# Performance work log

Hardware: AMD Instinct MI355X
Metric: run time of the kernel (lower is better)

The kernel has to match this reference:

```python
import jax, jax.numpy as jnp
import numpy as np

S, N, D, F = 32, 128, 256, 516
TRI = (N - 1) * N // 2  # fact(n-1) = n(n-1)/2 lower-triangular edge slots


def _mlp_readout(y, W0, b0, W1, b1, W2, b2):
    # standard MLPReadout with L=2 halving layers + final linear
    y = jax.nn.relu(y @ W0.T + b0)
    y = jax.nn.relu(y @ W1.T + b1)
    return y @ W2.T + b2


def _gru(xs, h0, Wih, Whh, bih, bhh):
    # xs: (S, T, Din); torch.nn.GRUCell math, scanned over time
    def step(h, x_t):
        gi = x_t @ Wih.T + bih
        gh = h @ Whh.T + bhh
        i_r, i_z, i_n = jnp.split(gi, 3, axis=-1)
        h_r, h_z, h_n = jnp.split(gh, 3, axis=-1)
        r = jax.nn.sigmoid(i_r + h_r)
        z = jax.nn.sigmoid(i_z + h_z)
        n = jnp.tanh(i_n + r * h_n)
        h_new = (1.0 - z) * n + z * h
        return h_new, h_new
    _, out = jax.lax.scan(step, h0, jnp.swapaxes(xs, 0, 1))
    return jnp.swapaxes(out, 0, 1)  # (S, T, D)


def setup_inputs() -> dict:
    key = jax.random.key(0)
    ks = jax.random.split(key, 16)
    def nrm(k, shape, s=0.05):
        return (jax.random.normal(k, shape) * s).astype(jnp.float32)
    return {
        'x': jax.random.uniform(ks[0], (S, N, F), dtype=jnp.float32),
        'con': jax.random.uniform(ks[1], (S, TRI, 2), dtype=jnp.float32),
        'z_ph': jax.random.uniform(ks[2], (D,), minval=-1.0, maxval=1.0, dtype=jnp.float32),
        'init_ph': jax.random.uniform(ks[3], (D,), minval=-1.0, maxval=1.0, dtype=jnp.float32),
        'cc_W0': nrm(ks[4], (D, 2 * D)), 'cc_b0': jnp.zeros((D,), jnp.float32),
        'cc_W1': nrm(ks[5], (D // 2, D)), 'cc_b1': jnp.zeros((D // 2,), jnp.float32),
        'cc_W2': nrm(ks[6], (D, D // 2)), 'cc_b2': jnp.zeros((D,), jnp.float32),
        'er_W0': nrm(ks[7], (D, 2 * D)), 'er_b0': jnp.zeros((D,), jnp.float32),
        'er_W1': nrm(ks[8], (D // 2, D)), 'er_b1': jnp.zeros((D // 2,), jnp.float32),
        'er_W2': nrm(ks[9], (2, D // 2)), 'er_b2': jnp.zeros((2,), jnp.float32),
        'rr_W': nrm(ks[10], (D, F)), 'rr_b': jnp.zeros((D,), jnp.float32),
        'dec_Wih': nrm(ks[11], (3 * D, D)), 'dec_Whh': nrm(ks[12], (3 * D, D)),
        'dec_bih': jnp.zeros((3 * D,), jnp.float32), 'dec_bhh': jnp.zeros((3 * D,), jnp.float32),
        'upd_Wih': nrm(ks[13], (3 * D, D)), 'upd_Whh': nrm(ks[14], (3 * D, D)),
        'upd_bih': jnp.zeros((3 * D,), jnp.float32), 'upd_bhh': jnp.zeros((3 * D,), jnp.float32),
    }


def reference(x, con, z_ph, init_ph, cc_W0, cc_b0, cc_W1, cc_b1, cc_W2, cc_b2,
              er_W0, er_b0, er_W1, er_b1, er_W2, er_b2, rr_W, rr_b,
              dec_Wih, dec_Whh, dec_bih, dec_bhh, upd_Wih, upd_Whh, upd_bih, upd_bhh):
    Sb = x.shape[0]
    Nm1 = x.shape[1] - 1
    # initial content = compact_content([z ; init]) (same for every sample)
    c0 = _mlp_readout(jnp.concatenate([z_ph, init_ph])[None, :],
                      cc_W0, cc_b0, cc_W1, cc_b1, cc_W2, cc_b2)
    c0 = jnp.broadcast_to(c0, (Sb, D))
    # update-model input stream depends only on data x[:, 1:] -> precompute
    rnninp = jax.nn.relu(jnp.einsum('snf,df->snd', x[:, 1:], rr_W) + rr_b)  # (S, N-1, D)
    h0 = jnp.zeros((Sb, D), x.dtype)
    u_out = _gru(rnninp, h0, upd_Wih, upd_Whh, upd_bih, upd_bhh)            # (S, N-1, D)
    # decoder consumes content0 then the first N-2 update outputs
    content_seq = jnp.concatenate([c0[:, None], u_out[:, :-1]], axis=1)     # (S, N-1, D)
    mem = _gru(content_seq, h0, dec_Wih, dec_Whh, dec_bih, dec_bhh)         # (S, N-1, D)
    # step i emits edges (j, i) for j <= i; flatten lower triangle (static indices)
    i_idx = np.repeat(np.arange(Nm1), np.arange(1, Nm1 + 1))
    j_idx = np.concatenate([np.arange(i + 1) for i in range(Nm1)])
    edge_rep = jnp.concatenate([mem[:, j_idx], mem[:, i_idx]], axis=-1)     # (S, TRI, 2D)
    logits = _mlp_readout(edge_rep, er_W0, er_b0, er_W1, er_b1, er_W2, er_b2)
    p = jax.nn.softmax(logits, axis=-1)                                     # (S, TRI, 2)
    # F.binary_cross_entropy with torch's log clamp at -100
    bce = -(con * jnp.clip(jnp.log(p), -100.0, None)
            + (1.0 - con) * jnp.clip(jnp.log1p(-p), -100.0, None))
    return jnp.sum(bce, axis=1)  # (S, 2) negative log-likelihood per class slot
```

## Files before the change

kernel.cpp:

```cpp
#include <hip/hip_runtime.h>
#include <cstddef>

#define S_ 32
#define NM1 127
#define D_ 256
#define F_ 516
#define TRI_ 8128
#define G_ 768
#define M_ (S_ * NM1)

typedef __bf16 v8bf __attribute__((ext_vector_type(8)));
typedef __bf16 bf2 __attribute__((ext_vector_type(2)));
typedef float v4f __attribute__((ext_vector_type(4)));

#if __has_builtin(__builtin_amdgcn_fdot2_f32_bf16)
#define HAS_DOT2 1
#else
#define HAS_DOT2 0
#endif

__device__ __forceinline__ unsigned short f2bf(float f) {
    unsigned int u = __float_as_uint(f);
    unsigned int r = (u + 0x7FFFu + ((u >> 16) & 1u)) >> 16;
    return (unsigned short)r;
}

__device__ __forceinline__ void store4bf(unsigned short* p, float4 v) {
    ushort4 q;
    q.x = f2bf(v.x); q.y = f2bf(v.y); q.z = f2bf(v.z); q.w = f2bf(v.w);
    *(ushort4*)p = q;
}

__device__ __forceinline__ bf2 u2bf2(unsigned int u) {
    union { unsigned int u; bf2 v; } x; x.u = u; return x.v;
}

__device__ __forceinline__ float bflo(unsigned int u) { return __uint_as_float(u << 16); }
__device__ __forceinline__ float bfhi(unsigned int u) { return __uint_as_float(u & 0xffff0000u); }

__device__ __forceinline__ float dot2bf(unsigned int w, unsigned int hh, float acc) {
#if HAS_DOT2
    return __builtin_amdgcn_fdot2_f32_bf16(u2bf2(w), u2bf2(hh), acc, false);
#else
    return acc + bflo(w) * bflo(hh) + bfhi(w) * bfhi(hh);
#endif
}

__device__ __forceinline__ float sigmoidf_(float x) { return 1.f / (1.f + __expf(-x)); }

__device__ __forceinline__ float fast_tanh(float x) {
    float ax = fabsf(x);
    float e = __expf(2.f * ax);
    float t = 1.f - 2.f / (e + 1.f);
    return copysignf(t, x);
}

__global__ __launch_bounds__(1024) void c0_kernel(
    const float* __restrict__ z_ph, const float* __restrict__ init_ph,
    const float* __restrict__ W0, const float* __restrict__ b0,
    const float* __restrict__ W1, const float* __restrict__ b1,
    const float* __restrict__ W2, const float* __restrict__ b2,
    float* __restrict__ c0_out, float* __restrict__ out_zero)
{
    __shared__ float v[512];
    __shared__ float h0[256];
    __shared__ float h1[128];
    __shared__ float red[4][256];
    __shared__ float red1[8][128];
    const int t = threadIdx.x;
    if (t < 512) v[t] = (t < 256) ? z_ph[t] : init_ph[t - 256];
    if (t < 64) out_zero[t] = 0.f;
    __syncthreads();
    {
        int row = t & 255, part = t >> 8;
        const float* w = W0 + (size_t)row * 512 + part * 128;
        const float* vv = v + part * 128;
        float a = 0.f;
        for (int k = 0; k < 128; ++k) a += w[k] * vv[k];
        red[part][row] = a;
    }
    __syncthreads();
    if (t < 256) {
        float a = b0[t] + red[0][t] + red[1][t] + red[2][t] + red[3][t];
        h0[t] = fmaxf(a, 0.f);
    }
    __syncthreads();
    {
        int row = t & 127, part = t >> 7;
        const float* w = W1 + (size_t)row * 256 + part * 32;
        const float* vv = h0 + part * 32;
        float a = 0.f;
        for (int k = 0; k < 32; ++k) a += w[k] * vv[k];
        red1[part][row] = a;
    }
    __syncthreads();
    if (t < 128) {
        float a = b1[t];
        for (int p = 0; p < 8; ++p) a += red1[p][t];
        h1[t] = fmaxf(a, 0.f);
    }
    __syncthreads();
    {
        int row = t & 255, part = t >> 8;
        const float* w = W2 + (size_t)row * 128 + part * 32;
        const float* vv = h1 + part * 32;
        float a = 0.f;
        for (int k = 0; k < 32; ++k) a += w[k] * vv[k];
        red[part][row] = a;
    }
    __syncthreads();
    if (t < 256) c0_out[t] = b2[t] + red[0][t] + red[1][t] + red[2][t] + red[3][t];
}

__device__ __forceinline__ void do_pack(const float* __restrict__ W,
                                        unsigned int* __restrict__ wpT, int idx)
{
    if (idx >= 128 * 768) return;
    int p = idx / 768, j = idx - p * 768;
    float a = W[(size_t)j * 256 + 2 * p];
    float b = W[(size_t)j * 256 + 2 * p + 1];
    wpT[idx] = (unsigned int)f2bf(a) | ((unsigned int)f2bf(b) << 16);
}

__device__ __forceinline__ void do_cvt(const float* __restrict__ src,
                                       unsigned short* __restrict__ dst,
                                       int idx, int N, int K, int lds_, int off, int ldd)
{
    if (idx >= N * ldd) return;
    int n = idx / ldd, k = idx - n * ldd;
    float v = (k < K) ? src[(size_t)n * lds_ + off + k] : 0.f;
    dst[idx] = f2bf(v);
}

#define PREP_BLOCKS 3464

__global__ __launch_bounds__(256) void prep_all(
    const float* __restrict__ upd_Whh, unsigned int* __restrict__ wpU,
    const float* __restrict__ dec_Whh, unsigned int* __restrict__ wpD,
    const float* __restrict__ rr_W, unsigned short* __restrict__ rwbf,
    const float* __restrict__ upd_Wih, unsigned short* __restrict__ uwbf,
    const float* __restrict__ dec_Wih, unsigned short* __restrict__ dwbf,
    const float* __restrict__ er_W0, unsigned short* __restrict__ w0bf,
    const float* __restrict__ er_W1, unsigned short* __restrict__ w1bf)
{
    int bid = blockIdx.x;
    const int tid = threadIdx.x;
    if (bid < 384) { do_pack(upd_Whh, wpU, bid * 256 + tid); return; }
    bid -= 384;
    if (bid < 384) { do_pack(dec_Whh, wpD, bid * 256 + tid); return; }
    bid -= 384;
    if (bid < 520) { do_cvt(rr_W, rwbf, bid * 256 + tid, 256, 516, 516, 0, 520); return; }
    bid -= 520;
    if (bid < 768) { do_cvt(upd_Wih, uwbf, bid * 256 + tid, 768, 256, 256, 0, 256); return; }
    bid -= 768;
    if (bid < 768) { do_cvt(dec_Wih, dwbf, bid * 256 + tid, 768, 256, 256, 0, 256); return; }
    bid -= 768;
    if (bid < 256) { do_cvt(er_W0, w0bf, bid * 256 + tid, 256, 256, 512, 0, 256); return; }
    bid -= 256;
    if (bid < 256) { do_cvt(er_W0, w0bf + 256 * 256, bid * 256 + tid, 256, 256, 512, 256, 256); return; }
    bid -= 256;
    do_cvt(er_W1, w1bf, bid * 256 + tid, 128, 256, 256, 0, 256);
}

__global__ __launch_bounds__(256) void gemm_mfma(
    const float* __restrict__ A, const unsigned short* __restrict__ B,
    const float* __restrict__ bias, const float* __restrict__ c0,
    float* __restrict__ C, float* __restrict__ C2,
    int M, int N, int K, int lda, int ldb, int mode, int act, int split)
{
    __shared__ __align__(16) unsigned short As[64 * 128];
    __shared__ __align__(16) unsigned short Bs[64 * 128];
    const int tid = threadIdx.x;
    const int m0 = blockIdx.x * 64, n0 = blockIdx.y * 64;
    const int wave = tid >> 6, lane = tid & 63;
    const int lr = lane & 15, quad = lane >> 4;

    v4f acc[4];
    const v4f z4 = {0.f, 0.f, 0.f, 0.f};
#pragma unroll
    for (int nt = 0; nt < 4; ++nt) acc[nt] = z4;

    for (int k0 = 0; k0 < K; k0 += 128) {
        for (int idx = tid; idx < 64 * 32; idx += 256) {
            int r = idx >> 5, kq = idx & 31;
            int k = k0 + kq * 4;
            int m = m0 + r; if (m > M - 1) m = M - 1;
            float4 a = {0.f, 0.f, 0.f, 0.f};
            if (k < K) {
                const float* Ar;
                if (mode == 1) {
                    int ss = m / 127, tt = m - ss * 127;
                    Ar = A + (size_t)(ss * 128 + tt + 1) * lda;
                } else if (mode == 2) {
                    int tt = m % 127;
                    Ar = (tt == 0) ? c0 : (A + (size_t)(m - 1) * lda);
                } else {
                    Ar = A + (size_t)m * lda;
                }
                a = *(const float4*)&Ar[k];
            }
            store4bf(&As[r * 128 + (((kq >> 1) ^ (r & 7)) << 3) + ((kq & 1) << 2)], a);
        }
        for (int idx = tid; idx < 64 * 16; idx += 256) {
            int c = idx >> 4, kb = idx & 15;
            int k = k0 + kb * 8;
            int n = n0 + c;
            uint4 bv = {0u, 0u, 0u, 0u};
            if (k < K) bv = *(const uint4*)&B[(size_t)n * ldb + k];
            *(uint4*)&Bs[c * 128 + ((kb ^ (c & 7)) << 3)] = bv;
        }
        __syncthreads();
        const int row = wave * 16 + lr;
        const int rem = K - k0;
        const int kkm = (rem >= 128) ? 4 : ((rem + 31) >> 5);
        for (int kk = 0; kk < kkm; ++kk) {
            const v8bf af = *(const v8bf*)&As[row * 128 + ((((kk << 2) + quad) ^ (row & 7)) << 3)];
#pragma unroll
            for (int nt = 0; nt < 4; ++nt) {
                const int col = nt * 16 + lr;
                const v8bf bf = *(const v8bf*)&Bs[col * 128 + ((((kk << 2) + quad) ^ (col & 7)) << 3)];
                acc[nt] = __builtin_amdgcn_mfma_f32_16x16x32_bf16(af, bf, acc[nt], 0, 0, 0);
            }
        }
        __syncthreads();
    }
#pragma unroll
    for (int nt = 0; nt < 4; ++nt) {
        const int col = n0 + nt * 16 + lr;
#pragma unroll
        for (int r = 0; r < 4; ++r) {
            const int row = m0 + wave * 16 + quad * 4 + r;
            if (row < M) {
                float v = acc[nt][r];
                if (split) {
                    if (col < 256) C[(size_t)row * 256 + col] = v;
                    else C2[(size_t)row * 256 + (col - 256)] = v + bias[col - 256];
                } else {
                    if (bias) v += bias[col];
                    if (act) v = fmaxf(v, 0.f);
                    C[(size_t)row * N + col] = v;
                }
            }
        }
    }
}

__global__ __launch_bounds__(768, 3) void gru_scan4(
    const float* __restrict__ gi, const unsigned int* __restrict__ wpT,
    const float* __restrict__ bhh, float* __restrict__ outp, int T)
{
    const int s = blockIdx.x, j = threadIdx.x;
    __shared__ unsigned int hb[2][128];
    __shared__ float dred[768];
    __shared__ float gns[256];

    unsigned int wh[64];
#pragma unroll
    for (int p = 0; p < 64; ++p) wh[p] = wpT[p * 768 + j];

    const float bj = bhh[j];
    const float* g0 = gi + (size_t)s * T * G_;
    float* o0 = outp + (size_t)s * T * D_;
    float g_cur = g0[j];
    float h = 0.f;
    if (j < 128) { hb[0][j] = 0u; hb[1][j] = 0u; }
    __syncthreads();

    for (int t = 0; t < T; ++t) {
        float g_next = 0.f;
        if (t + 1 < T) g_next = g0[(size_t)(t + 1) * G_ + j];

        unsigned int wsb[2][16];
#pragma unroll
        for (int i = 0; i < 16; ++i) wsb[0][i] = wpT[(64 + i) * 768 + j];

        const uint4* hq4 = (const uint4*)hb[t & 1];
        float a0 = 0.f, a1 = 0.f, a2 = 0.f, a3 = 0.f;
#pragma unroll
        for (int q = 0; q < 16; ++q) {
            uint4 hv = hq4[q];
            a0 = dot2bf(wh[4 * q + 0], hv.x, a0);
            a1 = dot2bf(wh[4 * q + 1], hv.y, a1);
            a2 = dot2bf(wh[4 * q + 2], hv.z, a2);
            a3 = dot2bf(wh[4 * q + 3], hv.w, a3);
        }
#pragma unroll
        for (int c = 0; c < 4; ++c) {
            if (c + 1 < 4) {
#pragma unroll
                for (int i = 0; i < 16; ++i)
                    wsb[(c + 1) & 1][i] = wpT[(64 + (c + 1) * 16 + i) * 768 + j];
            }
            const unsigned int* wc = wsb[c & 1];
#pragma unroll
            for (int qq = 0; qq < 4; ++qq) {
                uint4 hv = hq4[16 + c * 4 + qq];
                a0 = dot2bf(wc[4 * qq + 0], hv.x, a0);
                a1 = dot2bf(wc[4 * qq + 1], hv.y, a1);
                a2 = dot2bf(wc[4 * qq + 2], hv.z, a2);
                a3 = dot2bf(wc[4 * qq + 3], hv.w, a3);
            }
        }
        float a = (a0 + a1) + (a2 + a3) + bj;
        if (j < 512) {
            dred[j] = a + g_cur;
        } else {
            dred[j] = a;
            gns[j - 512] = g_cur;
        }
        __syncthreads();
        if (j < 256) {
            const float rg = sigmoidf_(dred[j]);
            const float zg = sigmoidf_(dred[256 + j]);
            const float ng = fast_tanh(gns[j] + rg * dred[512 + j]);
            const float hnew = ng + zg * (h - ng);
            h = hnew;
            o0[(size_t)t * D_ + j] = hnew;
            const float ho = __shfl_xor(hnew, 1);
            if ((j & 1) == 0)
                hb[(t + 1) & 1][j >> 1] =
                    (unsigned int)f2bf(hnew) | ((unsigned int)f2bf(ho) << 16);
        }
        g_cur = g_next;
        __syncthreads();
    }
}

__global__ __launch_bounds__(256) void edge_kernel(
    const float* __restrict__ Amat, const float* __restrict__ Bmat,
    const unsigned short* __restrict__ w1bf, const float* __restrict__ b1,
    const float* __restrict__ W2, const float* __restrict__ b2,
    const float* __restrict__ con, float* __restrict__ out)
{
    __shared__ __align__(16) unsigned short h1s[64 * 256];
    __shared__ int ijs[128];
    __shared__ float redw[4][2];
    const int tid = threadIdx.x;
    const int s = blockIdx.y;
    const int e0 = blockIdx.x * 64;

    if (tid < 64) {
        int e = e0 + tid;
        int i = (int)((sqrtf(8.f * (float)e + 1.f) - 1.f) * 0.5f);
        while (((i + 1) * (i + 2)) / 2 <= e) ++i;
        while ((i * (i + 1)) / 2 > e) --i;
        ijs[tid * 2] = i;
        ijs[tid * 2 + 1] = e - (i * (i + 1)) / 2;
    }
    __syncthreads();

    for (int idx = tid; idx < 64 * 64; idx += 256) {
        int e = idx >> 6, k4 = idx & 63;
        int i = ijs[e * 2], j = ijs[e * 2 + 1];
        float4 a = ((const float4*)(Amat + ((size_t)s * NM1 + j) * D_))[k4];
        float4 b = ((const float4*)(Bmat + ((size_t)s * NM1 + i) * D_))[k4];
        float4 hv;
        hv.x = fmaxf(a.x + b.x, 0.f);
        hv.y = fmaxf(a.y + b.y, 0.f);
        hv.z = fmaxf(a.z + b.z, 0.f);
        hv.w = fmaxf(a.w + b.w, 0.f);
        int pc = (k4 >> 1) ^ (e & 7);
        store4bf(&h1s[e * 256 + (pc << 3) + ((k4 & 1) << 2)], hv);
    }
    __syncthreads();

    const int wave = tid >> 6, lane = tid & 63;
    const int lr = lane & 15, quad = lane >> 4;
    const int row = wave * 16 + lr;

    v4f acc[8];
    const v4f vzero = {0.f, 0.f, 0.f, 0.f};
#pragma unroll
    for (int nt = 0; nt < 8; ++nt) acc[nt] = vzero;

#pragma unroll
    for (int kt = 0; kt < 8; ++kt) {
        const int c = kt * 4 + quad;
        const int pc = c ^ (row & 7);
        const v8bf afrag = *reinterpret_cast<const v8bf*>(&h1s[row * 256 + (pc << 3)]);
        const int ko = kt * 32 + quad * 8;
#pragma unroll
        for (int nt = 0; nt < 8; ++nt) {
            const v8bf bfrag = *reinterpret_cast<const v8bf*>(&w1bf[(size_t)(nt * 16 + lr) * D_ + ko]);
            acc[nt] = __builtin_amdgcn_mfma_f32_16x16x32_bf16(afrag, bfrag, acc[nt], 0, 0, 0);
        }
    }

    float w20[8], w21[8], b1v[8];
#pragma unroll
    for (int nt = 0; nt < 8; ++nt) {
        int oc = nt * 16 + lr;
        w20[nt] = W2[oc];
        w21[nt] = W2[128 + oc];
        b1v[nt] = b1[oc];
    }
    const float cb20 = b2[0], cb21 = b2[1];
    float bsum0 = 0.f, bsum1 = 0.f;
#pragma unroll
    for (int r = 0; r < 4; ++r) {
        float l0 = 0.f, l1 = 0.f;
#pragma unroll
        for (int nt = 0; nt < 8; ++nt) {
            float h2 = fmaxf(acc[nt][r] + b1v[nt], 0.f);
            l0 += h2 * w20[nt];
            l1 += h2 * w21[nt];
        }
#pragma unroll
        for (int d = 1; d < 16; d <<= 1) {
            l0 += __shfl_xor(l0, d);
            l1 += __shfl_xor(l1, d);
        }
        if (lr == 0) {
            int e = e0 + wave * 16 + quad * 4 + r;
            l0 += cb20; l1 += cb21;
            float mx = fmaxf(l0, l1);
            float lse = mx + logf(__expf(l0 - mx) + __expf(l1 - mx));
            float lp0 = fmaxf(l0 - lse, -100.f);
            float lp1 = fmaxf(l1 - lse, -100.f);
            float c0v = con[((size_t)s * TRI_ + e) * 2];
            float c1v = con[((size_t)s * TRI_ + e) * 2 + 1];
            bsum0 -= c0v * lp0 + (1.f - c0v) * lp1;
            bsum1 -= c1v * lp1 + (1.f - c1v) * lp0;
        }
    }
#pragma unroll
    for (int d = 1; d < 64; d <<= 1) {
        bsum0 += __shfl_xor(bsum0, d);
        bsum1 += __shfl_xor(bsum1, d);
    }
    if (lane == 0) { redw[wave][0] = bsum0; redw[wave][1] = bsum1; }
    __syncthreads();
    if (tid == 0) {
        float t0 = redw[0][0] + redw[1][0] + redw[2][0] + redw[3][0];
        float t1 = redw[0][1] + redw[1][1] + redw[2][1] + redw[3][1];
        atomicAdd(&out[s * 2], t0);
        atomicAdd(&out[s * 2 + 1], t1);
    }
}

extern "C" void kernel_launch(void* const* d_in, const int* in_sizes, int n_in,
                              void* d_out, int out_size, void* d_ws, size_t ws_size,
                              hipStream_t stream)
{
    (void)in_sizes; (void)n_in; (void)out_size; (void)ws_size;
    const float* x        = (const float*)d_in[0];
    const float* con      = (const float*)d_in[1];
    const float* z_ph     = (const float*)d_in[2];
    const float* init_ph  = (const float*)d_in[3];
    const float* cc_W0    = (const float*)d_in[4];
    const float* cc_b0    = (const float*)d_in[5];
    const float* cc_W1    = (const float*)d_in[6];
    const float* cc_b1    = (const float*)d_in[7];
    const float* cc_W2    = (const float*)d_in[8];
    const float* cc_b2    = (const float*)d_in[9];
    const float* er_W0    = (const float*)d_in[10];
    const float* er_b0    = (const float*)d_in[11];
    const float* er_W1    = (const float*)d_in[12];
    const float* er_b1    = (const float*)d_in[13];
    const float* er_W2    = (const float*)d_in[14];
    const float* er_b2    = (const float*)d_in[15];
    const float* rr_W     = (const float*)d_in[16];
    const float* rr_b     = (const float*)d_in[17];
    const float* dec_Wih  = (const float*)d_in[18];
    const float* dec_Whh  = (const float*)d_in[19];
    const float* dec_bih  = (const float*)d_in[20];
    const float* dec_bhh  = (const float*)d_in[21];
    const float* upd_Wih  = (const float*)d_in[22];
    const float* upd_Whh  = (const float*)d_in[23];
    const float* upd_bih  = (const float*)d_in[24];
    const float* upd_bhh  = (const float*)d_in[25];
    float* out = (float*)d_out;

    float* ws = (float*)d_ws;
    float* c0v  = ws;
    float* gi   = ws + 256;
    float* bufA = gi + (size_t)M_ * G_;
    float* bufB = bufA + (size_t)M_ * D_;
    float* memb = bufB + (size_t)M_ * D_;
    unsigned short* w1bf = (unsigned short*)(memb + (size_t)M_ * D_);
    unsigned int* wpU = (unsigned int*)(w1bf + 128 * 256);
    unsigned int* wpD = wpU + 128 * 768;
    unsigned short* rwbf = (unsigned short*)(wpD + 128 * 768);
    unsigned short* uwbf = rwbf + 256 * 520;
    unsigned short* dwbf = uwbf + 768 * 256;
    unsigned short* w0bf = dwbf + 768 * 256;

    c0_kernel<<<1, 1024, 0, stream>>>(z_ph, init_ph, cc_W0, cc_b0, cc_W1, cc_b1,
                                      cc_W2, cc_b2, c0v, out);
    prep_all<<<PREP_BLOCKS, 256, 0, stream>>>(upd_Whh, wpU, dec_Whh, wpD,
                                              rr_W, rwbf, upd_Wih, uwbf,
                                              dec_Wih, dwbf, er_W0, w0bf,
                                              er_W1, w1bf);
    gemm_mfma<<<dim3((M_ + 63) / 64, 256 / 64), 256, 0, stream>>>(
        x, rwbf, rr_b, nullptr, bufA, nullptr, M_, 256, 516, 516, 520, 1, 1, 0);
    gemm_mfma<<<dim3((M_ + 63) / 64, 768 / 64), 256, 0, stream>>>(
        bufA, uwbf, upd_bih, nullptr, gi, nullptr, M_, 768, 256, 256, 256, 0, 0, 0);
    gru_scan4<<<S_, 768, 0, stream>>>(gi, wpU, upd_bhh, bufB, NM1);
    gemm_mfma<<<dim3((M_ + 63) / 64, 768 / 64), 256, 0, stream>>>(
        bufB, dwbf, dec_bih, c0v, gi, nullptr, M_, 768, 256, 256, 256, 2, 0, 0);
    gru_scan4<<<S_, 768, 0, stream>>>(gi, wpD, dec_bhh, memb, NM1);
    gemm_mfma<<<dim3((M_ + 63) / 64, 512 / 64), 256, 0, stream>>>(
        memb, w0bf, er_b0, nullptr, bufA, bufB, M_, 512, 256, 256, 256, 0, 0, 1);
    edge_kernel<<<dim3(TRI_ / 64, S_), 256, 0, stream>>>(
        bufA, bufB, w1bf, er_b1, er_W2, er_b2, con, out);
}
```

Measured before the change: 714.8 us.

## Use MFMA for GRU recurrent matvec with register-resident fragment-packed weights

Rewrites the per-step hidden-state matvec in the GRU scan so it uses 16x16x32 bf16 MFMA instructions instead of per-thread dot2 loops. Only row 0 of the A operand carries real data; the other rows are broadcast copies of the same hidden vector. The recurrent weights are pre-packed into MFMA B-fragment layout and kept entirely in registers (48 uint4 per lane), which removes the per-step global weight streaming of the old version. The block shrinks from 768 to 512 threads, and biases plus input gates are added in the gate stage. In exchange, most of the MFMA work is wasted on redundant rows and register pressure is high.

```diff
diff --git a/kernel.cpp b/kernel.cpp
--- a/kernel.cpp
+++ b/kernel.cpp
@@ -10,14 +10,7 @@
 #define M_ (S_ * NM1)
 
 typedef __bf16 v8bf __attribute__((ext_vector_type(8)));
-typedef __bf16 bf2 __attribute__((ext_vector_type(2)));
 typedef float v4f __attribute__((ext_vector_type(4)));
-
-#if __has_builtin(__builtin_amdgcn_fdot2_f32_bf16)
-#define HAS_DOT2 1
-#else
-#define HAS_DOT2 0
-#endif
 
 __device__ __forceinline__ unsigned short f2bf(float f) {
     unsigned int u = __float_as_uint(f);
@@ -31,19 +24,8 @@
     *(ushort4*)p = q;
 }
 
-__device__ __forceinline__ bf2 u2bf2(unsigned int u) {
-    union { unsigned int u; bf2 v; } x; x.u = u; return x.v;
-}
-
-__device__ __forceinline__ float bflo(unsigned int u) { return __uint_as_float(u << 16); }
-__device__ __forceinline__ float bfhi(unsigned int u) { return __uint_as_float(u & 0xffff0000u); }
-
-__device__ __forceinline__ float dot2bf(unsigned int w, unsigned int hh, float acc) {
-#if HAS_DOT2
-    return __builtin_amdgcn_fdot2_f32_bf16(u2bf2(w), u2bf2(hh), acc, false);
-#else
-    return acc + bflo(w) * bflo(hh) + bfhi(w) * bfhi(hh);
-#endif
+__device__ __forceinline__ v8bf u4_to_v8bf(uint4 u) {
+    union { uint4 u; v8bf v; } x; x.u = u; return x.v;
 }
 
 __device__ __forceinline__ float sigmoidf_(float x) { return 1.f / (1.f + __expf(-x)); }
@@ -112,14 +94,22 @@
     if (t < 256) c0_out[t] = b2[t] + red[0][t] + red[1][t] + red[2][t] + red[3][t];
 }
 
-__device__ __forceinline__ void do_pack(const float* __restrict__ W,
-                                        unsigned int* __restrict__ wpT, int idx)
-{
-    if (idx >= 128 * 768) return;
-    int p = idx / 768, j = idx - p * 768;
-    float a = W[(size_t)j * 256 + 2 * p];
-    float b = W[(size_t)j * 256 + 2 * p + 1];
-    wpT[idx] = (unsigned int)f2bf(a) | ((unsigned int)f2bf(b) << 16);
+__device__ __forceinline__ void do_packfrag(const float* __restrict__ W,
+                                            uint4* __restrict__ wbuf, int idx)
+{
+    if (idx >= 48 * 8 * 64) return;
+    int ct = idx >> 9;
+    int rem = idx & 511;
+    int kk = rem >> 6;
+    int lane = rem & 63;
+    int lr = lane & 15, quad = lane >> 4;
+    const float* src = W + (size_t)(ct * 16 + lr) * 256 + kk * 32 + quad * 8;
+    unsigned int wd[4];
+#pragma unroll
+    for (int i = 0; i < 4; ++i)
+        wd[i] = (unsigned int)f2bf(src[2 * i]) | ((unsigned int)f2bf(src[2 * i + 1]) << 16);
+    uint4 v; v.x = wd[0]; v.y = wd[1]; v.z = wd[2]; v.w = wd[3];
+    wbuf[idx] = v;
 }
 
 __device__ __forceinline__ void do_cvt(const float* __restrict__ src,
@@ -132,11 +122,11 @@
     dst[idx] = f2bf(v);
 }
 
-#define PREP_BLOCKS 3464
+#define PREP_BLOCKS 2888
 
 __global__ __launch_bounds__(256) void prep_all(
-    const float* __restrict__ upd_Whh, unsigned int* __restrict__ wpU,
-    const float* __restrict__ dec_Whh, unsigned int* __restrict__ wpD,
+    const float* __restrict__ upd_Whh, uint4* __restrict__ wfU,
+    const float* __restrict__ dec_Whh, uint4* __restrict__ wfD,
     const float* __restrict__ rr_W, unsigned short* __restrict__ rwbf,
     const float* __restrict__ upd_Wih, unsigned short* __restrict__ uwbf,
     const float* __restrict__ dec_Wih, unsigned short* __restrict__ dwbf,
@@ -145,10 +135,10 @@
 {
     int bid = blockIdx.x;
     const int tid = threadIdx.x;
-    if (bid < 384) { do_pack(upd_Whh, wpU, bid * 256 + tid); return; }
-    bid -= 384;
-    if (bid < 384) { do_pack(dec_Whh, wpD, bid * 256 + tid); return; }
-    bid -= 384;
+    if (bid < 96) { do_packfrag(upd_Whh, wfU, bid * 256 + tid); return; }
+    bid -= 96;
+    if (bid < 96) { do_packfrag(dec_Whh, wfD, bid * 256 + tid); return; }
+    bid -= 96;
     if (bid < 520) { do_cvt(rr_W, rwbf, bid * 256 + tid, 256, 516, 516, 0, 520); return; }
     bid -= 520;
     if (bid < 768) { do_cvt(upd_Wih, uwbf, bid * 256 + tid, 768, 256, 256, 0, 256); return; }
@@ -245,83 +235,76 @@
     }
 }
 
-__global__ __launch_bounds__(768, 3) void gru_scan4(
-    const float* __restrict__ gi, const unsigned int* __restrict__ wpT,
+__global__ __launch_bounds__(512, 2) void gru_scan6(
+    const float* __restrict__ gi, const uint4* __restrict__ wf,
     const float* __restrict__ bhh, float* __restrict__ outp, int T)
 {
-    const int s = blockIdx.x, j = threadIdx.x;
-    __shared__ unsigned int hb[2][128];
+    const int s = blockIdx.x, tid = threadIdx.x;
+    const int w = tid >> 6, lane = tid & 63;
+    const int quad = lane >> 4;
+    __shared__ unsigned int hbuf[2][128];
     __shared__ float dred[768];
-    __shared__ float gns[256];
-
-    unsigned int wh[64];
-#pragma unroll
-    for (int p = 0; p < 64; ++p) wh[p] = wpT[p * 768 + j];
-
-    const float bj = bhh[j];
+
+    uint4 wfr[6][8];
+#pragma unroll
+    for (int c = 0; c < 6; ++c)
+#pragma unroll
+        for (int kk = 0; kk < 8; ++kk)
+            wfr[c][kk] = wf[((((w * 6 + c) * 8) + kk) << 6) | lane];
+
+    float br = 0.f, bz = 0.f, bn = 0.f;
+    float g_r = 0.f, g_z = 0.f, g_n = 0.f;
     const float* g0 = gi + (size_t)s * T * G_;
     float* o0 = outp + (size_t)s * T * D_;
-    float g_cur = g0[j];
     float h = 0.f;
-    if (j < 128) { hb[0][j] = 0u; hb[1][j] = 0u; }
+    if (tid < 256) {
+        br = bhh[tid]; bz = bhh[256 + tid]; bn = bhh[512 + tid];
+        g_r = g0[tid]; g_z = g0[256 + tid]; g_n = g0[512 + tid];
+    }
+    if (tid < 128) { hbuf[0][tid] = 0u; hbuf[1][tid] = 0u; }
+
+    v4f acc[6];
+    const v4f z4 = {0.f, 0.f, 0.f, 0.f};
+#pragma unroll
+    for (int c = 0; c < 6; ++c) acc[c] = z4;
     __syncthreads();
 
     for (int t = 0; t < T; ++t) {
-        float g_next = 0.f;
-        if (t + 1 < T) g_next = g0[(size_t)(t + 1) * G_ + j];
-
-        unsigned int wsb[2][16];
-#pragma unroll
-        for (int i = 0; i < 16; ++i) wsb[0][i] = wpT[(64 + i) * 768 + j];
-
-        const uint4* hq4 = (const uint4*)hb[t & 1];
-        float a0 = 0.f, a1 = 0.f, a2 = 0.f, a3 = 0.f;
-#pragma unroll
-        for (int q = 0; q < 16; ++q) {
-            uint4 hv = hq4[q];
-            a0 = dot2bf(wh[4 * q + 0], hv.x, a0);
-            a1 = dot2bf(wh[4 * q + 1], hv.y, a1);
-            a2 = dot2bf(wh[4 * q + 2], hv.z, a2);
-            a3 = dot2bf(wh[4 * q + 3], hv.w, a3);
-        }
-#pragma unroll
-        for (int c = 0; c < 4; ++c) {
-            if (c + 1 < 4) {
-#pragma unroll
-                for (int i = 0; i < 16; ++i)
-                    wsb[(c + 1) & 1][i] = wpT[(64 + (c + 1) * 16 + i) * 768 + j];
-            }
-            const unsigned int* wc = wsb[c & 1];
-#pragma unroll
-            for (int qq = 0; qq < 4; ++qq) {
-                uint4 hv = hq4[16 + c * 4 + qq];
-                a0 = dot2bf(wc[4 * qq + 0], hv.x, a0);
-                a1 = dot2bf(wc[4 * qq + 1], hv.y, a1);
-                a2 = dot2bf(wc[4 * qq + 2], hv.z, a2);
-                a3 = dot2bf(wc[4 * qq + 3], hv.w, a3);
-            }
-        }
-        float a = (a0 + a1) + (a2 + a3) + bj;
-        if (j < 512) {
-            dred[j] = a + g_cur;
-        } else {
-            dred[j] = a;
-            gns[j - 512] = g_cur;
-        }
+        float ngr = 0.f, ngz = 0.f, ngn = 0.f;
+        if (tid < 256 && t + 1 < T) {
+            const float* gn_ = g0 + (size_t)(t + 1) * G_;
+            ngr = gn_[tid]; ngz = gn_[256 + tid]; ngn = gn_[512 + tid];
+        }
+        const unsigned int* hq = hbuf[t & 1];
+#pragma unroll
+        for (int kk = 0; kk < 8; ++kk) {
+            const v8bf af = *(const v8bf*)&hq[kk * 16 + quad * 4];
+#pragma unroll
+            for (int c = 0; c < 6; ++c)
+                acc[c] = __builtin_amdgcn_mfma_f32_16x16x32_bf16(
+                    af, u4_to_v8bf(wfr[c][kk]), acc[c], 0, 0, 0);
+        }
+        if (lane < 16) {
+#pragma unroll
+            for (int c = 0; c < 6; ++c)
+                dred[(w * 6 + c) * 16 + lane] = acc[c][0];
+        }
+#pragma unroll
+        for (int c = 0; c < 6; ++c) acc[c] = z4;
         __syncthreads();
-        if (j < 256) {
-            const float rg = sigmoidf_(dred[j]);
-            const float zg = sigmoidf_(dred[256 + j]);
-            const float ng = fast_tanh(gns[j] + rg * dred[512 + j]);
+        if (tid < 256) {
+            const float rg = sigmoidf_(g_r + dred[tid] + br);
+            const float zg = sigmoidf_(g_z + dred[256 + tid] + bz);
+            const float ng = fast_tanh(g_n + rg * (dred[512 + tid] + bn));
             const float hnew = ng + zg * (h - ng);
             h = hnew;
-            o0[(size_t)t * D_ + j] = hnew;
+            o0[(size_t)t * D_ + tid] = hnew;
             const float ho = __shfl_xor(hnew, 1);
-            if ((j & 1) == 0)
-                hb[(t + 1) & 1][j >> 1] =
+            if ((tid & 1) == 0)
+                hbuf[(t + 1) & 1][tid >> 1] =
                     (unsigned int)f2bf(hnew) | ((unsigned int)f2bf(ho) << 16);
-        }
-        g_cur = g_next;
+            g_r = ngr; g_z = ngz; g_n = ngn;
+        }
         __syncthreads();
     }
 }
@@ -478,16 +461,16 @@
     float* bufB = bufA + (size_t)M_ * D_;
     float* memb = bufB + (size_t)M_ * D_;
     unsigned short* w1bf = (unsigned short*)(memb + (size_t)M_ * D_);
-    unsigned int* wpU = (unsigned int*)(w1bf + 128 * 256);
-    unsigned int* wpD = wpU + 128 * 768;
-    unsigned short* rwbf = (unsigned short*)(wpD + 128 * 768);
+    unsigned short* rwbf = w1bf + 128 * 256;
     unsigned short* uwbf = rwbf + 256 * 520;
     unsigned short* dwbf = uwbf + 768 * 256;
     unsigned short* w0bf = dwbf + 768 * 256;
+    uint4* wfU = (uint4*)(((size_t)(w0bf + 512 * 256) + 15) & ~(size_t)15);
+    uint4* wfD = wfU + 48 * 8 * 64;
 
     c0_kernel<<<1, 1024, 0, stream>>>(z_ph, init_ph, cc_W0, cc_b0, cc_W1, cc_b1,
                                       cc_W2, cc_b2, c0v, out);
-    prep_all<<<PREP_BLOCKS, 256, 0, stream>>>(upd_Whh, wpU, dec_Whh, wpD,
+    prep_all<<<PREP_BLOCKS, 256, 0, stream>>>(upd_Whh, wfU, dec_Whh, wfD,
                                               rr_W, rwbf, upd_Wih, uwbf,
                                               dec_Wih, dwbf, er_W0, w0bf,
                                               er_W1, w1bf);
@@ -495,10 +478,10 @@
         x, rwbf, rr_b, nullptr, bufA, nullptr, M_, 256, 516, 516, 520, 1, 1, 0);
     gemm_mfma<<<dim3((M_ + 63) / 64, 768 / 64), 256, 0, stream>>>(
         bufA, uwbf, upd_bih, nullptr, gi, nullptr, M_, 768, 256, 256, 256, 0, 0, 0);
-    gru_scan4<<<S_, 768, 0, stream>>>(gi, wpU, upd_bhh, bufB, NM1);
+    gru_scan6<<<S_, 512, 0, stream>>>(gi, wfU, upd_bhh, bufB, NM1);
     gemm_mfma<<<dim3((M_ + 63) / 64, 768 / 64), 256, 0, stream>>>(
         bufB, dwbf, dec_bih, c0v, gi, nullptr, M_, 768, 256, 256, 256, 2, 0, 0);
-    gru_scan4<<<S_, 768, 0, stream>>>(gi, wpD, dec_bhh, memb, NM1);
+    gru_scan6<<<S_, 512, 0, stream>>>(gi, wfD, dec_bhh, memb, NM1);
     gemm_mfma<<<dim3((M_ + 63) / 64, 512 / 64), 256, 0, stream>>>(
         memb, w0bf, er_b0, nullptr, bufA, bufB, M_, 512, 256, 256, 256, 0, 0, 1);
     edge_kernel<<<dim3(TRI_ / 64, S_), 256, 0, stream>>>(
```

Result: faster. 682.9 us (-4.5%).
